# Optimization experiments

Measured on AMD Instinct MI355X. Metric: run time of the kernel, lower is better.

The kernel has to match this reference:

```python
import jax, jax.numpy as jnp
import numpy as np

C = 768            # config.channels
CH, CW = 16, 16    # coarse span shape for group 'screen'
N = CH * CW        # total coarse positions = 256
FH, FW, FP = 16, 16, 2
F = FH * FW * FP   # fine_total = 512
K = 4              # top4 sample mode
B = 1024           # sb


def _ln(x, g, b, eps=1e-5):
    m = jnp.mean(x, axis=-1, keepdims=True)
    v = jnp.mean((x - m) ** 2, axis=-1, keepdims=True)
    return (x - m) / jnp.sqrt(v + eps) * g + b


def _mlp3(x, W1, b1, W2, b2, W3, b3):
    h = jax.nn.gelu(x @ W1 + b1)
    h = jax.nn.gelu(h @ W2 + b2)
    return h @ W3 + b3


def setup_inputs() -> dict:
    key = jax.random.key(0)
    ks = jax.random.split(key, 16)

    def w(k, fan_in, shape):
        return jax.random.normal(k, shape, jnp.float32) * (1.0 / np.sqrt(fan_in))

    return {
        "x": jax.random.normal(ks[0], (B, C), jnp.float32),
        "g_in": jnp.ones((C,), jnp.float32),
        "b_in": jnp.zeros((C,), jnp.float32),
        # coarse head: C -> C -> C -> N
        "cW1": w(ks[1], C, (C, C)), "cb1": jnp.zeros((C,), jnp.float32),
        "cW2": w(ks[2], C, (C, C)), "cb2": jnp.zeros((C,), jnp.float32),
        "cW3": w(ks[3], C, (C, N)), "cb3": jnp.zeros((N,), jnp.float32),
        # coarse embedding
        "emb": jax.random.normal(ks[4], (N, C), jnp.float32),
        "g_e": jnp.ones((C,), jnp.float32),
        "b_e": jnp.zeros((C,), jnp.float32),
        # fine head: 2C -> C -> C -> F
        "fW1": w(ks[5], 2 * C, (2 * C, C)), "fb1": jnp.zeros((C,), jnp.float32),
        "fW2": w(ks[6], C, (C, C)), "fb2": jnp.zeros((C,), jnp.float32),
        "fW3": w(ks[7], C, (C, F)), "fb3": jnp.zeros((F,), jnp.float32),
        # no-op head
        "nW": w(ks[8], C, (C, 1)), "nb": jnp.zeros((1,), jnp.float32),
    }


def reference(x, g_in, b_in, cW1, cb1, cW2, cb2, cW3, cb3, emb, g_e, b_e,
              fW1, fb1, fW2, fb2, fW3, fb3, nW, nb):
    b = x.shape[0]
    xn = _ln(x, g_in, b_in)                                   # (b, C)
    no_op = xn @ nW + nb                                      # (b, 1)
    coarse = _mlp3(xn, cW1, cb1, cW2, cb2, cW3, cb3)          # (b, N)

    # top4 routing
    _, i = jax.lax.top_k(coarse, K)                           # (b, K) int32
    e = _ln(emb[i], g_e, b_e)                                 # (b, K, C)
    fine_in = jnp.concatenate(
        [jnp.broadcast_to(xn[:, None, :], (b, K, C)), e], axis=-1)  # (b, K, 2C)
    fine = _mlp3(fine_in, fW1, fb1, fW2, fb2, fW3, fb3)       # (b, K, F)

    log_f = jnp.log(jnp.float32(F))
    xfull = jnp.broadcast_to(coarse[:, :, None], (b, N, F)) - log_f  # (b, N, F)
    upd = fine + log_f - jax.nn.logsumexp(fine, axis=-1, keepdims=True)
    xfull = xfull.at[jnp.arange(b)[:, None], i].add(upd)      # scatter-combine

    # per-group permute: (b, ch, cw, fh, fw, fp) -> (b, ch, fh, cw, fw, fp)
    xg = xfull.reshape(b, CH, CW, FH, FW, FP)
    xg = jnp.transpose(xg, (0, 1, 3, 2, 4, 5)).reshape(b, -1)
    return jnp.concatenate([no_op, xg], axis=-1)              # (b, 1 + N*F)
```

## Files before the change

### kernel.cpp

```cpp
#include <hip/hip_runtime.h>
#include <hip/hip_bf16.h>
#include <math.h>

typedef unsigned short u16;
typedef unsigned int   u32;
typedef __attribute__((ext_vector_type(8))) short s16x8;
typedef __attribute__((ext_vector_type(4))) float f32x4;

#define CB 768
#define NB 256
#define FB 512
#define BATCH 1024
#define OUTC 131073
#define LOGF 6.2383246250395077f

__device__ __forceinline__ u16 f2bf(float f){
    u32 u = __float_as_uint(f);
    u32 r = u + 0x7FFFu + ((u >> 16) & 1u);
    return (u16)(r >> 16);
}
__device__ __forceinline__ float bf2f(u16 s){ return __uint_as_float(((u32)s) << 16); }
__device__ __forceinline__ bool probe_bf(const void* g){ return ((const u16*)g)[0] == 0x3F80u; }
__device__ __forceinline__ float loadraw(const void* p, size_t i, bool isbf){
    return isbf ? bf2f(((const u16*)p)[i]) : ((const float*)p)[i];
}
__device__ __forceinline__ void split3(float f, u16& h, u16& l, u16& q){
    h = f2bf(f); float r1 = f - bf2f(h);
    l = f2bf(r1); float r2 = r1 - bf2f(l);
    q = f2bf(r2);
}
__device__ __forceinline__ float gelu_f(float x){
    return 0.5f * x * (1.0f + tanhf(0.7978845608028654f * (x + 0.044715f * x * x * x)));
}
__device__ __forceinline__ f32x4 mfma16x16x32(s16x8 a, s16x8 b, f32x4 c){
    return __builtin_amdgcn_mfma_f32_16x16x32_bf16(a, b, c, 0, 0, 0);
}

__device__ __forceinline__ float blockReduce(float v, float* sb, bool domax){
    #pragma unroll
    for (int o = 32; o > 0; o >>= 1){
        float ov = __shfl_down(v, o, 64);
        v = domax ? fmaxf(v, ov) : (v + ov);
    }
    int w = threadIdx.x >> 6, lane = threadIdx.x & 63;
    if (lane == 0) sb[w] = v;
    __syncthreads();
    float r = domax ? fmaxf(fmaxf(sb[0], sb[1]), fmaxf(sb[2], sb[3]))
                    : (sb[0] + sb[1] + sb[2] + sb[3]);
    __syncthreads();
    return r;
}

struct TransDesc { const void* src; u16* dh; u16* dl; int K; int N; int start; int tilesX; };
struct TD6 { TransDesc d[6]; };

#define T_TRANS 3456
#define T_LNEND 4480
#define T_CIEND 4496
#define T_GRID  4497

__global__ __launch_bounds__(256) void prep_k(TD6 td,
        const void* x, const void* g, const void* bb, const void* nW, const void* nb,
        const void* cb3, const void* ginp,
        u16* __restrict__ xh, u16* __restrict__ xl, u16* __restrict__ xq,
        float* __restrict__ noop, float* __restrict__ coarse, float* __restrict__ sumexp){
    __shared__ float t[32][33];
    __shared__ float sb[4];
    bool isbf = probe_bf(ginp);
    int blk = blockIdx.x, tid = threadIdx.x;
    if (blk < T_TRANS){
        int e = 0;
        #pragma unroll
        for (int i = 1; i < 6; i++) if (blk >= td.d[i].start) e = i;
        TransDesc d = td.d[e];
        int rel = blk - d.start;
        int n0 = (rel % d.tilesX) * 32;
        int k0 = (rel / d.tilesX) * 32;
        int tx = tid & 31, ty = tid >> 5;
        #pragma unroll
        for (int i = 0; i < 32; i += 8)
            t[ty + i][tx] = loadraw(d.src, (size_t)(k0 + ty + i) * d.N + n0 + tx, isbf);
        __syncthreads();
        #pragma unroll
        for (int i = 0; i < 32; i += 8){
            float f = t[tx][ty + i];
            u16 h = f2bf(f);
            d.dh[(size_t)(n0 + ty + i) * d.K + k0 + tx] = h;
            if (d.dl)
                d.dl[(size_t)(n0 + ty + i) * d.K + k0 + tx] = f2bf(f - bf2f(h));
        }
    } else if (blk < T_LNEND){
        int b = blk - T_TRANS;
        float v[3];
        #pragma unroll
        for (int i = 0; i < 3; i++) v[i] = loadraw(x, (size_t)b * CB + tid + i * 256, isbf);
        float mean = blockReduce(v[0] + v[1] + v[2], sb, false) * (1.0f / 768.0f);
        float d0 = v[0] - mean, d1 = v[1] - mean, d2 = v[2] - mean;
        float var = blockReduce(d0*d0 + d1*d1 + d2*d2, sb, false) * (1.0f / 768.0f);
        float inv = 1.0f / sqrtf(var + 1e-5f);
        float dot = 0.0f;
        #pragma unroll
        for (int i = 0; i < 3; i++){
            int c = tid + i * 256;
            float xi = (v[i] - mean) * inv * loadraw(g, c, isbf) + loadraw(bb, c, isbf);
            u16 h, l, q; split3(xi, h, l, q);
            size_t o = (size_t)b * CB + c;
            xh[o] = h; xl[o] = l; xq[o] = q;
            dot += xi * loadraw(nW, c, isbf);
        }
        dot = blockReduce(dot, sb, false);
        if (tid == 0) noop[b] = dot + loadraw(nb, 0, isbf);
    } else if (blk < T_CIEND){
        int base = (blk - T_LNEND) * 16384;
        #pragma unroll
        for (int j = 0; j < 64; j++){
            int i = base + j * 256 + tid;
            coarse[i] = loadraw(cb3, i & 255, isbf);
        }
    } else {
        #pragma unroll
        for (int j = 0; j < 16; j++) sumexp[j * 256 + tid] = 0.0f;
    }
}

template<int ASPLIT, int BSPLIT, int ACT, int OUTMODE>
__global__ __launch_bounds__(256) void gemm_k(
        const u16* __restrict__ Ah, const u16* __restrict__ Al, const u16* __restrict__ Aq,
        const u16* __restrict__ Bth, const u16* __restrict__ Btl,
        const void* __restrict__ bias, const void* __restrict__ ginp,
        void* __restrict__ o0, void* __restrict__ o1, void* __restrict__ o2,
        int M, int N, int K){
    constexpr int LDA = 40;
    __shared__ u16 As[ASPLIT][128 * LDA];
    __shared__ u16 Bs[BSPLIT][64 * LDA];
    bool isbf = probe_bf(ginp);
    const int m0 = blockIdx.y * 128, n0 = blockIdx.x * 64;
    const int tid = threadIdx.x;
    const int w = tid >> 6, lane = tid & 63, lm = lane & 15, q = lane >> 4;
    const int kc = K / gridDim.z;
    const int kbeg = blockIdx.z * kc, kend = kbeg + kc;
    f32x4 acc[2][4];
    #pragma unroll
    for (int i = 0; i < 2; i++)
        #pragma unroll
        for (int j = 0; j < 4; j++) acc[i][j] = (f32x4)(0.0f);
    const int ar = tid >> 1, ac = (tid & 1) * 16;
    const int bn = tid >> 2, bc = (tid & 3) * 8;

    s16x8 pa[ASPLIT][2], pb[BSPLIT];
    auto load_regs = [&](int kk){
        const u16* s0 = Ah + (size_t)(m0 + ar) * K + kk + ac;
        pa[0][0] = *(const s16x8*)(s0);
        pa[0][1] = *(const s16x8*)(s0 + 8);
        if (ASPLIT == 3){
            const u16* s1 = Al + (size_t)(m0 + ar) * K + kk + ac;
            pa[1][0] = *(const s16x8*)(s1);
            pa[1][1] = *(const s16x8*)(s1 + 8);
            const u16* s2 = Aq + (size_t)(m0 + ar) * K + kk + ac;
            pa[2][0] = *(const s16x8*)(s2);
            pa[2][1] = *(const s16x8*)(s2 + 8);
        }
        pb[0] = *(const s16x8*)(Bth + (size_t)(n0 + bn) * K + kk + bc);
        if (BSPLIT == 2)
            pb[1] = *(const s16x8*)(Btl + (size_t)(n0 + bn) * K + kk + bc);
    };

    load_regs(kbeg);
    for (int k0 = kbeg; k0 < kend; k0 += 32){
        __syncthreads();
        #pragma unroll
        for (int s = 0; s < ASPLIT; s++){
            *(s16x8*)&As[s][ar*LDA + ac]     = pa[s][0];
            *(s16x8*)&As[s][ar*LDA + ac + 8] = pa[s][1];
        }
        #pragma unroll
        for (int s = 0; s < BSPLIT; s++)
            *(s16x8*)&Bs[s][bn*LDA + bc] = pb[s];
        __syncthreads();
        if (k0 + 32 < kend) load_regs(k0 + 32);

        s16x8 afr[ASPLIT][2], bfr[BSPLIT][4];
        #pragma unroll
        for (int mt = 0; mt < 2; mt++)
            #pragma unroll
            for (int s = 0; s < ASPLIT; s++)
                afr[s][mt] = *(const s16x8*)&As[s][(w*32 + mt*16 + lm)*LDA + q*8];
        #pragma unroll
        for (int nt = 0; nt < 4; nt++)
            #pragma unroll
            for (int s = 0; s < BSPLIT; s++)
                bfr[s][nt] = *(const s16x8*)&Bs[s][(nt*16 + lm)*LDA + q*8];
        #pragma unroll
        for (int mt = 0; mt < 2; mt++)
            #pragma unroll
            for (int nt = 0; nt < 4; nt++){
                acc[mt][nt] = mfma16x16x32(afr[0][mt], bfr[0][nt], acc[mt][nt]);
                if (ASPLIT == 3){
                    acc[mt][nt] = mfma16x16x32(afr[1][mt], bfr[0][nt], acc[mt][nt]);
                    acc[mt][nt] = mfma16x16x32(afr[2][mt], bfr[0][nt], acc[mt][nt]);
                }
                if (BSPLIT == 2){
                    acc[mt][nt] = mfma16x16x32(afr[0][mt], bfr[1][nt], acc[mt][nt]);
                    if (ASPLIT == 3)
                        acc[mt][nt] = mfma16x16x32(afr[1][mt], bfr[1][nt], acc[mt][nt]);
                }
            }
    }

    if (OUTMODE == 3){
        #pragma unroll
        for (int nt = 0; nt < 4; nt++){
            int n = n0 + nt*16 + lm;
            #pragma unroll
            for (int mt = 0; mt < 2; mt++)
                #pragma unroll
                for (int r = 0; r < 4; r++){
                    int m = m0 + w*32 + mt*16 + q*4 + r;
                    atomicAdd(&((float*)o0)[(size_t)m * N + n], acc[mt][nt][r]);
                }
        }
    } else if (OUTMODE == 4){
        #pragma unroll
        for (int mt = 0; mt < 2; mt++)
            #pragma unroll
            for (int r = 0; r < 4; r++){
                int m = m0 + w*32 + mt*16 + q*4 + r;
                float esum = 0.0f;
                #pragma unroll
                for (int nt = 0; nt < 4; nt++){
                    int n = n0 + nt*16 + lm;
                    float vv = acc[mt][nt][r] + loadraw(bias, n, isbf);
                    ((float*)o0)[(size_t)m * N + n] = vv;
                    esum += expf(vv);
                }
                #pragma unroll
                for (int o = 8; o > 0; o >>= 1) esum += __shfl_down(esum, o, 16);
                if (lm == 0) atomicAdd(&((float*)o1)[m], esum);
            }
    } else {
        #pragma unroll
        for (int nt = 0; nt < 4; nt++){
            int n = n0 + nt*16 + lm;
            float bv = loadraw(bias, n, isbf);
            #pragma unroll
            for (int mt = 0; mt < 2; mt++){
                #pragma unroll
                for (int r = 0; r < 4; r++){
                    int m = m0 + w*32 + mt*16 + q*4 + r;
                    float vv = acc[mt][nt][r] + bv;
                    if (ACT == 1) vv = gelu_f(vv);
                    size_t o = (size_t)m * N + n;
                    if (OUTMODE == 0)      ((float*)o0)[o] = vv;
                    else if (OUTMODE == 1) ((u16*)o0)[o] = f2bf(vv);
                    else {
                        u16 h, l, qq; split3(vv, h, l, qq);
                        ((u16*)o0)[o] = h; ((u16*)o1)[o] = l; ((u16*)o2)[o] = qq;
                    }
                }
            }
        }
    }
}

__global__ __launch_bounds__(256) void topkfine_k(const float* __restrict__ coarse,
        const void* __restrict__ emb, const void* __restrict__ ge, const void* __restrict__ be,
        const void* __restrict__ ginp, const u16* __restrict__ xh,
        u16* __restrict__ fin, unsigned char* __restrict__ ksel){
    __shared__ float sb[4];
    __shared__ float swv[4]; __shared__ int swi[4];
    __shared__ int sel4[4]; __shared__ int chosen_s;
    bool isbf = probe_bf(ginp);
    int b = blockIdx.x, tid = threadIdx.x;
    int w = tid >> 6, lane = tid & 63;
    float v = coarse[(size_t)b * NB + tid];
    ksel[(size_t)b * NB + tid] = (unsigned char)255;
    __syncthreads();
    for (int k = 0; k < 4; k++){
        float bv = v; int bi = tid;
        #pragma unroll
        for (int o = 32; o > 0; o >>= 1){
            float ov = __shfl_xor(bv, o, 64);
            int   oi = __shfl_xor(bi, o, 64);
            if (ov > bv || (ov == bv && oi < bi)){ bv = ov; bi = oi; }
        }
        if (lane == 0){ swv[w] = bv; swi[w] = bi; }
        __syncthreads();
        if (tid == 0){
            float cv = swv[0]; int ci = swi[0];
            #pragma unroll
            for (int j = 1; j < 4; j++)
                if (swv[j] > cv || (swv[j] == cv && swi[j] < ci)){ cv = swv[j]; ci = swi[j]; }
            sel4[k] = ci; chosen_s = ci;
            ksel[(size_t)b * NB + ci] = (unsigned char)k;
        }
        __syncthreads();
        if (tid == chosen_s) v = -INFINITY;
    }
    #pragma unroll 1
    for (int k = 0; k < 4; k++){
        int n = sel4[k];
        float vv[3];
        #pragma unroll
        for (int i = 0; i < 3; i++) vv[i] = loadraw(emb, (size_t)n * CB + tid + i * 256, isbf);
        float mean = blockReduce(vv[0] + vv[1] + vv[2], sb, false) * (1.0f / 768.0f);
        float d0 = vv[0] - mean, d1 = vv[1] - mean, d2 = vv[2] - mean;
        float var = blockReduce(d0*d0 + d1*d1 + d2*d2, sb, false) * (1.0f / 768.0f);
        float inv = 1.0f / sqrtf(var + 1e-5f);
        u16* dst = fin + ((size_t)b * 4 + k) * (2 * CB);
        #pragma unroll
        for (int i = 0; i < 3; i++){
            int c = tid + i * 256;
            dst[c] = xh[(size_t)b * CB + c];
            dst[CB + c] = f2bf((vv[i] - mean) * inv * loadraw(ge, c, isbf) + loadraw(be, c, isbf));
        }
    }
}

__global__ __launch_bounds__(256) void out_k(const float* __restrict__ coarse,
        const float* __restrict__ fine, const float* __restrict__ sumexp,
        const unsigned char* __restrict__ ksel, const float* __restrict__ noop,
        const void* __restrict__ ginp, void* __restrict__ outp){
    u32 g0 = ((u32)blockIdx.x * 256u + (u32)threadIdx.x) * 8u;
    const u32 total = (u32)BATCH * (u32)OUTC;
    if (g0 >= total) return;
    bool isbf = probe_bf(ginp);
    float vals[8];
    #pragma unroll
    for (int e = 0; e < 8; e++){
        u32 gg = g0 + (u32)e;
        u32 qq = gg >> 17;
        int rr = (int)(gg & 131071u) - (int)qq;
        if (rr < 0){ qq -= 1u; rr += 131073; }
        int b = (int)qq;
        float val;
        if (rr == 0){
            val = noop[b];
        } else {
            int j = rr - 1;
            int ch = j >> 13;
            int rem = j & 8191;
            int fh = rem >> 9, cw = (rem >> 5) & 15, ff = rem & 31;
            int n = (ch << 4) + cw;
            val = coarse[(size_t)b * NB + n] - LOGF;
            int ks = ksel[(size_t)b * NB + n];
            if (ks != 255){
                int fr = b * 4 + ks;
                val += fine[((size_t)fr << 9) + (fh << 5) + ff] + (LOGF - logf(sumexp[fr]));
            }
        }
        vals[e] = val;
    }
    if (isbf){
        u16 res[8];
        #pragma unroll
        for (int e = 0; e < 8; e++) res[e] = f2bf(vals[e]);
        *(s16x8*)((u16*)outp + g0) = *(s16x8*)res;
    } else {
        float* of = (float*)outp + g0;
        *(float4*)(of)     = make_float4(vals[0], vals[1], vals[2], vals[3]);
        *(float4*)(of + 4) = make_float4(vals[4], vals[5], vals[6], vals[7]);
    }
}

extern "C" void kernel_launch(void* const* d_in, const int* in_sizes, int n_in,
                              void* d_out, int out_size, void* d_ws, size_t ws_size,
                              hipStream_t stream){
    (void)in_sizes; (void)n_in; (void)out_size; (void)ws_size;
    char* ws = (char*)d_ws;
    size_t off = 0;
    auto alloc = [&](size_t bytes){ void* p = ws + off; off += (bytes + 255) & ~(size_t)255; return p; };

    u16* xh  = (u16*)alloc((size_t)1024*768*2);
    u16* xl  = (u16*)alloc((size_t)1024*768*2);
    u16* xq  = (u16*)alloc((size_t)1024*768*2);
    u16* h1h = (u16*)alloc((size_t)1024*768*2);
    u16* h1l = (u16*)alloc((size_t)1024*768*2);
    u16* h1q = (u16*)alloc((size_t)1024*768*2);
    u16* h2h = (u16*)alloc((size_t)1024*768*2);
    u16* h2l = (u16*)alloc((size_t)1024*768*2);
    u16* h2q = (u16*)alloc((size_t)1024*768*2);
    float* coarse = (float*)alloc((size_t)1024*256*4);
    unsigned char* ksel = (unsigned char*)alloc((size_t)1024*256);
    float* noop   = (float*)alloc((size_t)1024*4);
    float* sumexp = (float*)alloc((size_t)4096*4);
    u16*   fin    = (u16*)  alloc((size_t)4096*1536*2);
    u16*   gg1    = (u16*)  alloc((size_t)4096*768*2);
    u16*   gg2    = (u16*)  alloc((size_t)4096*768*2);
    float* fine   = (float*)alloc((size_t)4096*512*4);
    u16* cW1th = (u16*)alloc((size_t)768*768*2);
    u16* cW1tl = (u16*)alloc((size_t)768*768*2);
    u16* cW2th = (u16*)alloc((size_t)768*768*2);
    u16* cW2tl = (u16*)alloc((size_t)768*768*2);
    u16* cW3th = (u16*)alloc((size_t)768*256*2);
    u16* cW3tl = (u16*)alloc((size_t)768*256*2);
    u16* fW1t  = (u16*)alloc((size_t)1536*768*2);
    u16* fW2t  = (u16*)alloc((size_t)768*768*2);
    u16* fW3t  = (u16*)alloc((size_t)768*512*2);

    const void* ginp = d_in[1];

    TD6 td;
    td.d[0] = { d_in[3],  cW1th, cW1tl,  768, 768,    0, 24 };
    td.d[1] = { d_in[5],  cW2th, cW2tl,  768, 768,  576, 24 };
    td.d[2] = { d_in[7],  cW3th, cW3tl,  768, 256, 1152,  8 };
    td.d[3] = { d_in[12], fW1t,  nullptr,1536, 768, 1344, 24 };
    td.d[4] = { d_in[14], fW2t,  nullptr, 768, 768, 2496, 24 };
    td.d[5] = { d_in[16], fW3t,  nullptr, 768, 512, 3072, 16 };

    prep_k<<<T_GRID, 256, 0, stream>>>(td, d_in[0], d_in[1], d_in[2], d_in[18], d_in[19],
                                       d_in[8], ginp, xh, xl, xq, noop, coarse, sumexp);

    gemm_k<3,2,1,2><<<dim3(12, 8, 1), 256, 0, stream>>>(xh, xl, xq, cW1th, cW1tl,
            d_in[4], ginp, h1h, h1l, h1q, 1024, 768, 768);
    gemm_k<3,2,1,2><<<dim3(12, 8, 1), 256, 0, stream>>>(h1h, h1l, h1q, cW2th, cW2tl,
            d_in[6], ginp, h2h, h2l, h2q, 1024, 768, 768);
    gemm_k<3,2,0,3><<<dim3( 4, 8, 6), 256, 0, stream>>>(h2h, h2l, h2q, cW3th, cW3tl,
            nullptr, ginp, coarse, nullptr, nullptr, 1024, 256, 768);

    topkfine_k<<<1024, 256, 0, stream>>>(coarse, d_in[9], d_in[10], d_in[11], ginp, xh, fin, ksel);

    gemm_k<1,1,1,1><<<dim3(12, 32, 1), 256, 0, stream>>>(fin, nullptr, nullptr, fW1t, nullptr,
            d_in[13], ginp, gg1, nullptr, nullptr, 4096, 768, 1536);
    gemm_k<1,1,1,1><<<dim3(12, 32, 1), 256, 0, stream>>>(gg1, nullptr, nullptr, fW2t, nullptr,
            d_in[15], ginp, gg2, nullptr, nullptr, 4096, 768, 768);
    gemm_k<1,1,0,4><<<dim3( 8, 32, 1), 256, 0, stream>>>(gg2, nullptr, nullptr, fW3t, nullptr,
            d_in[17], ginp, fine, sumexp, nullptr, 4096, 512, 768);

    u32 total_chunks = ((u32)BATCH * (u32)OUTC) / 8u;
    u32 blocks = (total_chunks + 255u) / 256u;
    out_k<<<blocks, 256, 0, stream>>>(coarse, fine, sumexp, ksel, noop, ginp, d_out);
}
```

Measured before the change: 815.9 us.

## Parameterize GEMM tile shape per launch and split top-k embedding work across blocks

Templates the MFMA GEMM on its tile dimensions (TM, TN) and uses a 2x2 warp layout. The coarse GEMMs switch to 64x64 tiles to launch more blocks, and the fine GEMMs use 128x128 tiles for more operand reuse. The top-k/embedding-LN kernel now runs four blocks per row, one per selected index, with each block recomputing the top-4 selection. The aim is better occupancy on the small coarse GEMMs and less global traffic on the large fine GEMMs, at the cost of redundant top-k work and higher register pressure in the larger tiles.

```diff
diff --git a/kernel.cpp b/kernel.cpp
--- a/kernel.cpp
+++ b/kernel.cpp
@@ -123,7 +123,7 @@
     }
 }
 
-template<int ASPLIT, int BSPLIT, int ACT, int OUTMODE>
+template<int ASPLIT, int BSPLIT, int ACT, int OUTMODE, int TM, int TN>
 __global__ __launch_bounds__(256) void gemm_k(
         const u16* __restrict__ Ah, const u16* __restrict__ Al, const u16* __restrict__ Aq,
         const u16* __restrict__ Bth, const u16* __restrict__ Btl,
@@ -131,38 +131,45 @@
         void* __restrict__ o0, void* __restrict__ o1, void* __restrict__ o2,
         int M, int N, int K){
     constexpr int LDA = 40;
-    __shared__ u16 As[ASPLIT][128 * LDA];
-    __shared__ u16 Bs[BSPLIT][64 * LDA];
+    constexpr int MT = TM / 32;
+    constexpr int NT = TN / 32;
+    constexpr int APT = (TM == 128) ? 2 : 1;
+    constexpr int BPT = (TN == 128) ? 2 : 1;
+    __shared__ u16 As[ASPLIT][TM * LDA];
+    __shared__ u16 Bs[BSPLIT][TN * LDA];
     bool isbf = probe_bf(ginp);
-    const int m0 = blockIdx.y * 128, n0 = blockIdx.x * 64;
+    const int m0 = blockIdx.y * TM, n0 = blockIdx.x * TN;
     const int tid = threadIdx.x;
     const int w = tid >> 6, lane = tid & 63, lm = lane & 15, q = lane >> 4;
+    const int wr = w & 1, wc = w >> 1;
     const int kc = K / gridDim.z;
     const int kbeg = blockIdx.z * kc, kend = kbeg + kc;
-    f32x4 acc[2][4];
+    f32x4 acc[MT][NT];
     #pragma unroll
-    for (int i = 0; i < 2; i++)
-        #pragma unroll
-        for (int j = 0; j < 4; j++) acc[i][j] = (f32x4)(0.0f);
-    const int ar = tid >> 1, ac = (tid & 1) * 16;
-    const int bn = tid >> 2, bc = (tid & 3) * 8;
-
-    s16x8 pa[ASPLIT][2], pb[BSPLIT];
+    for (int i = 0; i < MT; i++)
+        #pragma unroll
+        for (int j = 0; j < NT; j++) acc[i][j] = (f32x4)(0.0f);
+    const int ar = (TM == 128) ? (tid >> 1) : (tid >> 2);
+    const int ac = (TM == 128) ? ((tid & 1) * 16) : ((tid & 3) * 8);
+    const int bn = (TN == 128) ? (tid >> 1) : (tid >> 2);
+    const int bc = (TN == 128) ? ((tid & 1) * 16) : ((tid & 3) * 8);
+    const u16* Apl[3] = { Ah, Al, Aq };
+    const u16* Bpl[2] = { Bth, Btl };
+
+    s16x8 pa[ASPLIT][APT], pb[BSPLIT][BPT];
     auto load_regs = [&](int kk){
-        const u16* s0 = Ah + (size_t)(m0 + ar) * K + kk + ac;
-        pa[0][0] = *(const s16x8*)(s0);
-        pa[0][1] = *(const s16x8*)(s0 + 8);
-        if (ASPLIT == 3){
-            const u16* s1 = Al + (size_t)(m0 + ar) * K + kk + ac;
-            pa[1][0] = *(const s16x8*)(s1);
-            pa[1][1] = *(const s16x8*)(s1 + 8);
-            const u16* s2 = Aq + (size_t)(m0 + ar) * K + kk + ac;
-            pa[2][0] = *(const s16x8*)(s2);
-            pa[2][1] = *(const s16x8*)(s2 + 8);
-        }
-        pb[0] = *(const s16x8*)(Bth + (size_t)(n0 + bn) * K + kk + bc);
-        if (BSPLIT == 2)
-            pb[1] = *(const s16x8*)(Btl + (size_t)(n0 + bn) * K + kk + bc);
+        #pragma unroll
+        for (int s = 0; s < ASPLIT; s++){
+            const u16* sp = Apl[s] + (size_t)(m0 + ar) * K + kk + ac;
+            pa[s][0] = *(const s16x8*)(sp);
+            if (APT == 2) pa[s][1] = *(const s16x8*)(sp + 8);
+        }
+        #pragma unroll
+        for (int s = 0; s < BSPLIT; s++){
+            const u16* sp = Bpl[s] + (size_t)(n0 + bn) * K + kk + bc;
+            pb[s][0] = *(const s16x8*)(sp);
+            if (BPT == 2) pb[s][1] = *(const s16x8*)(sp + 8);
+        }
     };
 
     load_regs(kbeg);
@@ -170,30 +177,32 @@
         __syncthreads();
         #pragma unroll
         for (int s = 0; s < ASPLIT; s++){
-            *(s16x8*)&As[s][ar*LDA + ac]     = pa[s][0];
-            *(s16x8*)&As[s][ar*LDA + ac + 8] = pa[s][1];
-        }
-        #pragma unroll
-        for (int s = 0; s < BSPLIT; s++)
-            *(s16x8*)&Bs[s][bn*LDA + bc] = pb[s];
+            *(s16x8*)&As[s][ar*LDA + ac] = pa[s][0];
+            if (APT == 2) *(s16x8*)&As[s][ar*LDA + ac + 8] = pa[s][1];
+        }
+        #pragma unroll
+        for (int s = 0; s < BSPLIT; s++){
+            *(s16x8*)&Bs[s][bn*LDA + bc] = pb[s][0];
+            if (BPT == 2) *(s16x8*)&Bs[s][bn*LDA + bc + 8] = pb[s][1];
+        }
         __syncthreads();
         if (k0 + 32 < kend) load_regs(k0 + 32);
 
-        s16x8 afr[ASPLIT][2], bfr[BSPLIT][4];
-        #pragma unroll
-        for (int mt = 0; mt < 2; mt++)
+        s16x8 afr[ASPLIT][MT], bfr[BSPLIT][NT];
+        #pragma unroll
+        for (int mt = 0; mt < MT; mt++)
             #pragma unroll
             for (int s = 0; s < ASPLIT; s++)
-                afr[s][mt] = *(const s16x8*)&As[s][(w*32 + mt*16 + lm)*LDA + q*8];
-        #pragma unroll
-        for (int nt = 0; nt < 4; nt++)
+                afr[s][mt] = *(const s16x8*)&As[s][((mt*2 + wr)*16 + lm)*LDA + q*8];
+        #pragma unroll
+        for (int nt = 0; nt < NT; nt++)
             #pragma unroll
             for (int s = 0; s < BSPLIT; s++)
-                bfr[s][nt] = *(const s16x8*)&Bs[s][(nt*16 + lm)*LDA + q*8];
-        #pragma unroll
-        for (int mt = 0; mt < 2; mt++)
-            #pragma unroll
-            for (int nt = 0; nt < 4; nt++){
+                bfr[s][nt] = *(const s16x8*)&Bs[s][((nt*2 + wc)*16 + lm)*LDA + q*8];
+        #pragma unroll
+        for (int mt = 0; mt < MT; mt++)
+            #pragma unroll
+            for (int nt = 0; nt < NT; nt++){
                 acc[mt][nt] = mfma16x16x32(afr[0][mt], bfr[0][nt], acc[mt][nt]);
                 if (ASPLIT == 3){
                     acc[mt][nt] = mfma16x16x32(afr[1][mt], bfr[0][nt], acc[mt][nt]);
@@ -209,26 +218,26 @@
 
     if (OUTMODE == 3){
         #pragma unroll
-        for (int nt = 0; nt < 4; nt++){
-            int n = n0 + nt*16 + lm;
-            #pragma unroll
-            for (int mt = 0; mt < 2; mt++)
+        for (int nt = 0; nt < NT; nt++){
+            int n = n0 + (nt*2 + wc)*16 + lm;
+            #pragma unroll
+            for (int mt = 0; mt < MT; mt++)
                 #pragma unroll
                 for (int r = 0; r < 4; r++){
-                    int m = m0 + w*32 + mt*16 + q*4 + r;
+                    int m = m0 + (mt*2 + wr)*16 + q*4 + r;
                     atomicAdd(&((float*)o0)[(size_t)m * N + n], acc[mt][nt][r]);
                 }
         }
     } else if (OUTMODE == 4){
         #pragma unroll
-        for (int mt = 0; mt < 2; mt++)
+        for (int mt = 0; mt < MT; mt++)
             #pragma unroll
             for (int r = 0; r < 4; r++){
-                int m = m0 + w*32 + mt*16 + q*4 + r;
+                int m = m0 + (mt*2 + wr)*16 + q*4 + r;
                 float esum = 0.0f;
                 #pragma unroll
-                for (int nt = 0; nt < 4; nt++){
-                    int n = n0 + nt*16 + lm;
+                for (int nt = 0; nt < NT; nt++){
+                    int n = n0 + (nt*2 + wc)*16 + lm;
                     float vv = acc[mt][nt][r] + loadraw(bias, n, isbf);
                     ((float*)o0)[(size_t)m * N + n] = vv;
                     esum += expf(vv);
@@ -239,14 +248,14 @@
             }
     } else {
         #pragma unroll
-        for (int nt = 0; nt < 4; nt++){
-            int n = n0 + nt*16 + lm;
+        for (int nt = 0; nt < NT; nt++){
+            int n = n0 + (nt*2 + wc)*16 + lm;
             float bv = loadraw(bias, n, isbf);
             #pragma unroll
-            for (int mt = 0; mt < 2; mt++){
+            for (int mt = 0; mt < MT; mt++){
                 #pragma unroll
                 for (int r = 0; r < 4; r++){
-                    int m = m0 + w*32 + mt*16 + q*4 + r;
+                    int m = m0 + (mt*2 + wr)*16 + q*4 + r;
                     float vv = acc[mt][nt][r] + bv;
                     if (ACT == 1) vv = gelu_f(vv);
                     size_t o = (size_t)m * N + n;
@@ -270,10 +279,11 @@
     __shared__ float swv[4]; __shared__ int swi[4];
     __shared__ int sel4[4]; __shared__ int chosen_s;
     bool isbf = probe_bf(ginp);
-    int b = blockIdx.x, tid = threadIdx.x;
+    int bk = blockIdx.x, tid = threadIdx.x;
+    int b = bk >> 2, kk = bk & 3;
     int w = tid >> 6, lane = tid & 63;
     float v = coarse[(size_t)b * NB + tid];
-    ksel[(size_t)b * NB + tid] = (unsigned char)255;
+    if (kk == 0) ksel[(size_t)b * NB + tid] = (unsigned char)255;
     __syncthreads();
     for (int k = 0; k < 4; k++){
         float bv = v; int bi = tid;
@@ -291,28 +301,28 @@
             for (int j = 1; j < 4; j++)
                 if (swv[j] > cv || (swv[j] == cv && swi[j] < ci)){ cv = swv[j]; ci = swi[j]; }
             sel4[k] = ci; chosen_s = ci;
-            ksel[(size_t)b * NB + ci] = (unsigned char)k;
         }
         __syncthreads();
         if (tid == chosen_s) v = -INFINITY;
     }
-    #pragma unroll 1
-    for (int k = 0; k < 4; k++){
-        int n = sel4[k];
-        float vv[3];
-        #pragma unroll
-        for (int i = 0; i < 3; i++) vv[i] = loadraw(emb, (size_t)n * CB + tid + i * 256, isbf);
-        float mean = blockReduce(vv[0] + vv[1] + vv[2], sb, false) * (1.0f / 768.0f);
-        float d0 = vv[0] - mean, d1 = vv[1] - mean, d2 = vv[2] - mean;
-        float var = blockReduce(d0*d0 + d1*d1 + d2*d2, sb, false) * (1.0f / 768.0f);
-        float inv = 1.0f / sqrtf(var + 1e-5f);
-        u16* dst = fin + ((size_t)b * 4 + k) * (2 * CB);
-        #pragma unroll
-        for (int i = 0; i < 3; i++){
-            int c = tid + i * 256;
-            dst[c] = xh[(size_t)b * CB + c];
-            dst[CB + c] = f2bf((vv[i] - mean) * inv * loadraw(ge, c, isbf) + loadraw(be, c, isbf));
-        }
+    if (kk == 0 && tid == 0){
+        #pragma unroll
+        for (int j = 0; j < 4; j++) ksel[(size_t)b * NB + sel4[j]] = (unsigned char)j;
+    }
+    int n = sel4[kk];
+    float vv[3];
+    #pragma unroll
+    for (int i = 0; i < 3; i++) vv[i] = loadraw(emb, (size_t)n * CB + tid + i * 256, isbf);
+    float mean = blockReduce(vv[0] + vv[1] + vv[2], sb, false) * (1.0f / 768.0f);
+    float d0 = vv[0] - mean, d1 = vv[1] - mean, d2 = vv[2] - mean;
+    float var = blockReduce(d0*d0 + d1*d1 + d2*d2, sb, false) * (1.0f / 768.0f);
+    float inv = 1.0f / sqrtf(var + 1e-5f);
+    u16* dst = fin + ((size_t)b * 4 + kk) * (2 * CB);
+    #pragma unroll
+    for (int i = 0; i < 3; i++){
+        int c = tid + i * 256;
+        dst[c] = xh[(size_t)b * CB + c];
+        dst[CB + c] = f2bf((vv[i] - mean) * inv * loadraw(ge, c, isbf) + loadraw(be, c, isbf));
     }
 }
 
@@ -410,20 +420,20 @@
     prep_k<<<T_GRID, 256, 0, stream>>>(td, d_in[0], d_in[1], d_in[2], d_in[18], d_in[19],
                                        d_in[8], ginp, xh, xl, xq, noop, coarse, sumexp);
 
-    gemm_k<3,2,1,2><<<dim3(12, 8, 1), 256, 0, stream>>>(xh, xl, xq, cW1th, cW1tl,
+    gemm_k<3,2,1,2,64,64><<<dim3(12, 16, 1), 256, 0, stream>>>(xh, xl, xq, cW1th, cW1tl,
             d_in[4], ginp, h1h, h1l, h1q, 1024, 768, 768);
-    gemm_k<3,2,1,2><<<dim3(12, 8, 1), 256, 0, stream>>>(h1h, h1l, h1q, cW2th, cW2tl,
+    gemm_k<3,2,1,2,64,64><<<dim3(12, 16, 1), 256, 0, stream>>>(h1h, h1l, h1q, cW2th, cW2tl,
             d_in[6], ginp, h2h, h2l, h2q, 1024, 768, 768);
-    gemm_k<3,2,0,3><<<dim3( 4, 8, 6), 256, 0, stream>>>(h2h, h2l, h2q, cW3th, cW3tl,
+    gemm_k<3,2,0,3,64,64><<<dim3( 4, 16, 3), 256, 0, stream>>>(h2h, h2l, h2q, cW3th, cW3tl,
             nullptr, ginp, coarse, nullptr, nullptr, 1024, 256, 768);
 
-    topkfine_k<<<1024, 256, 0, stream>>>(coarse, d_in[9], d_in[10], d_in[11], ginp, xh, fin, ksel);
-
-    gemm_k<1,1,1,1><<<dim3(12, 32, 1), 256, 0, stream>>>(fin, nullptr, nullptr, fW1t, nullptr,
+    topkfine_k<<<4096, 256, 0, stream>>>(coarse, d_in[9], d_in[10], d_in[11], ginp, xh, fin, ksel);
+
+    gemm_k<1,1,1,1,128,128><<<dim3(6, 32, 1), 256, 0, stream>>>(fin, nullptr, nullptr, fW1t, nullptr,
             d_in[13], ginp, gg1, nullptr, nullptr, 4096, 768, 1536);
-    gemm_k<1,1,1,1><<<dim3(12, 32, 1), 256, 0, stream>>>(gg1, nullptr, nullptr, fW2t, nullptr,
+    gemm_k<1,1,1,1,128,128><<<dim3(6, 32, 1), 256, 0, stream>>>(gg1, nullptr, nullptr, fW2t, nullptr,
             d_in[15], ginp, gg2, nullptr, nullptr, 4096, 768, 768);
-    gemm_k<1,1,0,4><<<dim3( 8, 32, 1), 256, 0, stream>>>(gg2, nullptr, nullptr, fW3t, nullptr,
+    gemm_k<1,1,0,4,128,64><<<dim3(8, 32, 1), 256, 0, stream>>>(gg2, nullptr, nullptr, fW3t, nullptr,
             d_in[17], ginp, fine, sumexp, nullptr, 4096, 512, 768);
 
     u32 total_chunks = ((u32)BATCH * (u32)OUTC) / 8u;
```

After: 813.0 us. About the same (-0.4%).
